# Optimization experiments

Measured on AMD Instinct MI355X. Metric: run time of the kernel, lower is better.

The kernel has to match this reference:

```python
import jax, jax.numpy as jnp
import numpy as np

D_MODEL = 1024
NUM_HEADS = 16
HEAD_DIM = D_MODEL // NUM_HEADS


def setup_inputs() -> dict:
    key = jax.random.key(0)
    ks = jax.random.split(key, 9)
    s = 1.0 / np.sqrt(D_MODEL)  # torch Linear default init range scale
    def lin(k):
        kw, kb = jax.random.split(k)
        W = jax.random.uniform(kw, (D_MODEL, D_MODEL), jnp.float32, -s, s)
        b = jax.random.uniform(kb, (D_MODEL,), jnp.float32, -s, s)
        return W, b
    Wq, bq = lin(ks[0])
    Wk, bk = lin(ks[1])
    Wv, bv = lin(ks[2])
    Wo, bo = lin(ks[3])
    x = jax.random.normal(ks[4], (4, 2048, D_MODEL), jnp.float32)
    return {"x": x, "Wq": Wq, "bq": bq, "Wk": Wk, "bk": bk,
            "Wv": Wv, "bv": bv, "Wo": Wo, "bo": bo}


def reference(x, Wq, bq, Wk, bk, Wv, bv, Wo, bo):
    B, S, _ = x.shape
    H, Dh = NUM_HEADS, HEAD_DIM
    scale = Dh ** -0.5
    # projections; W stored as [in, out] so y = x @ W + b
    q = (x @ Wq + bq).reshape(B, S, H, Dh).transpose(0, 2, 1, 3)  # [B,H,S,Dh]
    k = (x @ Wk + bk).reshape(B, S, H, Dh).transpose(0, 2, 1, 3)
    v = (x @ Wv + bv).reshape(B, S, H, Dh).transpose(0, 2, 1, 3)
    scores = jnp.einsum('bhqd,bhkd->bhqk', q, k) * scale  # [B,H,S,S]
    causal = jnp.tril(jnp.ones((S, S), dtype=bool))
    scores = jnp.where(causal[None, None], scores, jnp.finfo(scores.dtype).min)
    attn = jax.nn.softmax(scores, axis=-1)
    out = jnp.einsum('bhqk,bhkd->bhqd', attn, v)  # [B,H,S,Dh]
    out = out.transpose(0, 2, 1, 3).reshape(B, S, H * Dh)
    return out @ Wo + bo
```

## Files before the change

### kernel.cpp

```cpp
#include <hip/hip_runtime.h>
#include <math.h>

#define DM 1024
#define NH 16
#define DH 64
#define BB 4
#define SS 2048
#define MROWS (BB*SS)

typedef __bf16 bf16;
typedef __bf16 bf16x2 __attribute__((ext_vector_type(2)));
typedef __bf16 bf16x8 __attribute__((ext_vector_type(8)));
typedef float floatx4 __attribute__((ext_vector_type(4)));
typedef float floatx16 __attribute__((ext_vector_type(16)));
typedef unsigned int uintx4 __attribute__((ext_vector_type(4)));
typedef unsigned int uintx2 __attribute__((ext_vector_type(2)));

#if __has_builtin(__builtin_amdgcn_exp2f)
#define EXP2F __builtin_amdgcn_exp2f
#else
#define EXP2F exp2f
#endif

#define QSCALE (0.125f * 1.44269504088896f)

__device__ __forceinline__ void cp16(void* lds, const void* g) {
  __builtin_amdgcn_global_load_lds(
      (__attribute__((address_space(1))) void*)(void*)g,
      (__attribute__((address_space(3))) void*)lds,
      16, 0, 0);
}

__device__ __forceinline__ unsigned pk2(float a, float b) {
  bf16x2 t;
  t[0] = (bf16)a;
  t[1] = (bf16)b;
  return __builtin_bit_cast(unsigned, t);
}

#if __has_builtin(__builtin_amdgcn_permlane32_swap)
__device__ __forceinline__ void pl32(unsigned& a, unsigned& b) {
  uintx2 r = __builtin_amdgcn_permlane32_swap(a, b, false, false);
  a = r[0]; b = r[1];
}
#else
__device__ __forceinline__ void pl32(unsigned& a, unsigned& b) {
  asm volatile("v_permlane32_swap_b32 %0, %1" : "+v"(a), "+v"(b));
}
#endif

__global__ __launch_bounds__(256) void cvt_x(
    const float* __restrict__ X, bf16* __restrict__ Y) {
  int i = (blockIdx.x * 256 + threadIdx.x) * 8;
  float4 a = *(const float4*)&X[i];
  float4 b = *(const float4*)&X[i + 4];
  bf16x8 o;
  o[0] = (bf16)a.x; o[1] = (bf16)a.y; o[2] = (bf16)a.z; o[3] = (bf16)a.w;
  o[4] = (bf16)b.x; o[5] = (bf16)b.y; o[6] = (bf16)b.z; o[7] = (bf16)b.w;
  *(bf16x8*)&Y[i] = o;
}

__global__ __launch_bounds__(1024) void wtransc(
    const float* __restrict__ W0, const float* __restrict__ W1,
    const float* __restrict__ W2, const float* __restrict__ W3,
    bf16* __restrict__ T0, bf16* __restrict__ T1,
    bf16* __restrict__ T2, bf16* __restrict__ T3) {
  __shared__ float tile[32][33];
  const float* W; bf16* T;
  int z = blockIdx.z;
  if (z == 0)      { W = W0; T = T0; }
  else if (z == 1) { W = W1; T = T1; }
  else if (z == 2) { W = W2; T = T2; }
  else             { W = W3; T = T3; }
  int tx = threadIdx.x, ty = threadIdx.y;
  tile[ty][tx] = W[(blockIdx.y * 32 + ty) * DM + blockIdx.x * 32 + tx];
  __syncthreads();
  T[(blockIdx.x * 32 + ty) * DM + blockIdx.y * 32 + tx] = (bf16)tile[tx][ty];
}

#define BK 32

__global__ __launch_bounds__(512, 1) void gemm_qkv(
    const bf16* __restrict__ A, const bf16* __restrict__ WT,
    const float* __restrict__ bq, const float* __restrict__ bk,
    const float* __restrict__ bv,
    bf16* __restrict__ qb, bf16* __restrict__ kb, bf16* __restrict__ vt) {
  __shared__ __align__(16) char smem[(2 * 256 * 64 + 2 * 128 * 64) * 2];
  bf16* Ab = (bf16*)smem;
  bf16* Bb = (bf16*)(smem + 2 * 256 * 64 * 2);
  bf16* Ts = (bf16*)smem;

  int tid = threadIdx.x;
  int lane = tid & 63, w = tid >> 6;
  int wr = w >> 1, wc = w & 1;
  int qd = lane >> 4, l15 = lane & 15;

  int bid = blockIdx.x;
  int wg = (bid & 7) * 96 + (bid >> 3);
  int mb = wg / 24, nb = wg % 24;
  int m0 = mb * 256;
  int n0 = nb * 128;
  int which = n0 >> 10;

  floatx4 acc[4][4] = {};

  auto stageA = [&](int pb, int t, int hf) {
    for (int i = 0; i < 2; ++i) {
      int L = i * 512 + tid;
      int row = L >> 3, ch = L & 7;
      int sch = ch ^ (row & 7);
      cp16(&Ab[pb * 256 * 64 + (hf * 128 + row) * 64 + ch * 8],
           &A[(size_t)(m0 + hf * 128 + row) * DM + t * 64 + sch * 8]);
    }
  };
  auto stageB = [&](int pb, int t) {
    for (int i = 0; i < 2; ++i) {
      int L = i * 512 + tid;
      int row = L >> 3, ch = L & 7;
      int sch = ch ^ (row & 7);
      cp16(&Bb[pb * 128 * 64 + row * 64 + ch * 8],
           &WT[(size_t)(n0 + row) * DM + t * 64 + sch * 8]);
    }
  };
  auto ldA = [&](int pb, int mt, int ks) -> bf16x8 {
    int row = wr * 64 + mt * 16 + l15;
    int c = ((ks << 2) + qd) ^ (row & 7);
    return *(const bf16x8*)&Ab[pb * 256 * 64 + row * 64 + c * 8];
  };
  auto ldB = [&](int pb, int nt, int ks) -> bf16x8 {
    int row = wc * 64 + nt * 16 + l15;
    int c = ((ks << 2) + qd) ^ (row & 7);
    return *(const bf16x8*)&Bb[pb * 128 * 64 + row * 64 + c * 8];
  };

  stageA(0, 0, 0);
  stageA(0, 0, 1);
  stageB(0, 0);
  stageB(1, 1);
  asm volatile("s_waitcnt vmcnt(2)" ::: "memory");
  __builtin_amdgcn_s_barrier();

  for (int g = 0; g < 16; ++g) {
    int pb = g & 1;
    bf16x8 af0[2][2], bfr[4][2];
    for (int mt = 0; mt < 2; ++mt)
      for (int ks = 0; ks < 2; ++ks) af0[mt][ks] = ldA(pb, mt, ks);
    for (int nt = 0; nt < 4; ++nt)
      for (int ks = 0; ks < 2; ++ks) bfr[nt][ks] = ldB(pb, nt, ks);
    if (g + 1 < 16) { stageA(pb ^ 1, g + 1, 0); stageA(pb ^ 1, g + 1, 1); }
    __builtin_amdgcn_s_barrier();
    asm volatile("s_waitcnt lgkmcnt(0)" ::: "memory");
    __builtin_amdgcn_sched_barrier(0);
    __builtin_amdgcn_s_setprio(1);
    for (int mt = 0; mt < 2; ++mt)
      for (int nt = 0; nt < 4; ++nt)
        for (int ks = 0; ks < 2; ++ks)
          acc[mt][nt] = __builtin_amdgcn_mfma_f32_16x16x32_bf16(
              af0[mt][ks], bfr[nt][ks], acc[mt][nt], 0, 0, 0);
    __builtin_amdgcn_s_setprio(0);
    __builtin_amdgcn_s_barrier();
    bf16x8 af1[2][2];
    for (int mt = 0; mt < 2; ++mt)
      for (int ks = 0; ks < 2; ++ks) af1[mt][ks] = ldA(pb, 2 + mt, ks);
    if (g + 2 < 16) stageB(pb, g + 2);
    __builtin_amdgcn_s_barrier();
    asm volatile("s_waitcnt lgkmcnt(0)" ::: "memory");
    __builtin_amdgcn_sched_barrier(0);
    __builtin_amdgcn_s_setprio(1);
    for (int mt = 0; mt < 2; ++mt)
      for (int nt = 0; nt < 4; ++nt)
        for (int ks = 0; ks < 2; ++ks)
          acc[2 + mt][nt] = __builtin_amdgcn_mfma_f32_16x16x32_bf16(
              af1[mt][ks], bfr[nt][ks], acc[2 + mt][nt], 0, 0, 0);
    __builtin_amdgcn_s_setprio(0);
    if (g < 14)
      asm volatile("s_waitcnt vmcnt(2)" ::: "memory");
    else if (g == 14)
      asm volatile("s_waitcnt vmcnt(0)" ::: "memory");
    __builtin_amdgcn_s_barrier();
  }

  __syncthreads();

  const float* bias = (which == 0) ? bq : (which == 1) ? bk : bv;

  if (which == 2) {
    for (int nt = 0; nt < 4; ++nt) {
      int dl = wc * 64 + nt * 16 + l15;
      float bv_ = bias[(n0 & 1023) + dl];
      for (int mt = 0; mt < 4; ++mt)
        for (int r = 0; r < 4; ++r)
          Ts[dl * 264 + wr * 64 + mt * 16 + qd * 4 + r] =
              (bf16)(acc[mt][nt][r] + bv_);
    }
    __syncthreads();
    int dl = tid >> 2, s0 = (tid & 3) * 64;
    size_t vrow = (size_t)((n0 & 1023) + dl) * MROWS + m0 + s0;
    for (int j = 0; j < 8; ++j)
      *(bf16x8*)&vt[vrow + j * 8] = *(const bf16x8*)&Ts[dl * 264 + s0 + j * 8];
  } else {
    bf16* out = (which == 0) ? qb : kb;
    float sc = (which == 0) ? QSCALE : 1.0f;
    for (int nt = 0; nt < 4; ++nt) {
      int col = (n0 & 1023) + wc * 64 + nt * 16 + l15;
      float bv_ = bias[col];
      for (int mt = 0; mt < 4; ++mt)
        for (int r = 0; r < 4; ++r) {
          int row = m0 + wr * 64 + mt * 16 + qd * 4 + r;
          out[(size_t)row * DM + col] = (bf16)((acc[mt][nt][r] + bv_) * sc);
        }
    }
  }
}

__global__ __launch_bounds__(256, 4) void gemm_out(
    const bf16* __restrict__ A, const bf16* __restrict__ WT,
    const float* __restrict__ bias, float* __restrict__ C) {
  __shared__ __align__(16) bf16 As[2][64 * BK];
  __shared__ __align__(16) bf16 Bs[2][128 * BK];
  int tid = threadIdx.x;
  int lane = tid & 63, w = tid >> 6;
  int wm = (w >> 1) * 32;
  int wn = (w & 1) * 64;
  int m0 = blockIdx.x * 64;
  int n0 = blockIdx.y * 128;
  int qd = lane >> 4;
  int l15 = lane & 15;

  floatx4 acc[2][4] = {};

  auto stage = [&](int pb, int k0) {
    {
      int ci = w * 64;
      int c = ci + lane;
      int r = c >> 2, cc = (c & 3) * 8;
      cp16(&As[pb][ci * 8], &A[(size_t)(m0 + r) * DM + k0 + cc]);
    }
    for (int i = 0; i < 2; ++i) {
      int ci = (w * 2 + i) * 64;
      int c = ci + lane;
      int r = c >> 2, cc = (c & 3) * 8;
      cp16(&Bs[pb][ci * 8], &WT[(size_t)(n0 + r) * DM + k0 + cc]);
    }
  };

  stage(0, 0);
  __syncthreads();

  for (int t = 0; t < DM / BK; ++t) {
    int pb = t & 1;
    if (t + 1 < DM / BK) stage(pb ^ 1, (t + 1) * BK);
    bf16x8 af[2], bfr[4];
    for (int mt = 0; mt < 2; ++mt)
      af[mt] = *(const bf16x8*)&As[pb][(wm + mt * 16 + l15) * BK + qd * 8];
    for (int nt = 0; nt < 4; ++nt)
      bfr[nt] = *(const bf16x8*)&Bs[pb][(wn + nt * 16 + l15) * BK + qd * 8];
    for (int mt = 0; mt < 2; ++mt)
      for (int nt = 0; nt < 4; ++nt)
        acc[mt][nt] = __builtin_amdgcn_mfma_f32_16x16x32_bf16(
            af[mt], bfr[nt], acc[mt][nt], 0, 0, 0);
    __syncthreads();
  }

  for (int nt = 0; nt < 4; ++nt) {
    int col = n0 + wn + nt * 16 + l15;
    float bv = bias[col];
    for (int mt = 0; mt < 2; ++mt)
      for (int r = 0; r < 4; ++r) {
        int row = m0 + wm + mt * 16 + qd * 4 + r;
        C[(size_t)row * DM + col] = acc[mt][nt][r] + bv;
      }
  }
}

__global__ __launch_bounds__(256, 2) void attn_fwd(
    const bf16* __restrict__ Qg, const bf16* __restrict__ Kg,
    const bf16* __restrict__ Vt, bf16* __restrict__ O) {
  __shared__ __align__(16) bf16 Kbuf[3][64 * 64];
  __shared__ __align__(16) bf16 Vbuf[3][64 * 64];

  int tid = threadIdx.x;
  int lane = tid & 63, w = tid >> 6;
  int q31 = lane & 31, hi = lane >> 5;
  int pair = blockIdx.x, h = blockIdx.y, b = blockIdx.z;
  int base = b * SS;
  int hoff = h * DH;

  auto stage = [&](int bi, int kt) {
    int kbase = base + kt * 64;
    for (int i = 0; i < 2; ++i) {
      int c = i * 256 + tid;
      int row = c >> 3;
      int sch = (c & 7) ^ (row & 7);
      cp16(&Kbuf[bi][c * 8], &Kg[(size_t)(kbase + row) * DM + hoff + sch * 8]);
      cp16(&Vbuf[bi][c * 8],
           &Vt[(size_t)(hoff + row) * MROWS + base + kt * 64 + sch * 8]);
    }
  };

  int swz = q31 & 7;

  for (int ph = 0; ph < 2; ++ph) {
    int jt = ph ? (15 - pair) : pair;
    int q0 = jt * 128;
    int nkt = 2 * jt + 2;

    stage(0, 0);
    stage(1, 1);

    int rowq = q0 + w * 32 + q31;
    bf16x8 qf[4];
    for (int ds = 0; ds < 4; ++ds)
      qf[ds] = *(const bf16x8*)
          &Qg[(size_t)(base + rowq) * DM + hoff + ds * 16 + hi * 8];

    float lacc = 0.0f;
    floatx16 oacc0 = {}, oacc1 = {};

    asm volatile("s_waitcnt vmcnt(8)" ::: "memory");
    __builtin_amdgcn_s_barrier();

    int bi = 0;
    for (int kt = 0; kt < nkt; ++kt) {
      if (kt + 2 < nkt) stage((bi + 2) % 3, kt + 2);

      floatx16 sA = {}, sB = {};
      __builtin_amdgcn_s_setprio(1);
      for (int ds = 0; ds < 4; ++ds) {
        bf16x8 kfA = *(const bf16x8*)
            &Kbuf[bi][(q31)*64 + (((ds << 1) + hi) ^ swz) * 8];
        bf16x8 kfB = *(const bf16x8*)
            &Kbuf[bi][(32 + q31) * 64 + (((ds << 1) + hi) ^ swz) * 8];
        sA = __builtin_amdgcn_mfma_f32_32x32x16_bf16(kfA, qf[ds], sA, 0, 0, 0);
        sB = __builtin_amdgcn_mfma_f32_32x32x16_bf16(kfB, qf[ds], sB, 0, 0, 0);
      }
      __builtin_amdgcn_s_setprio(0);

      if (kt >= 2 * jt) {
#pragma unroll
        for (int r = 0; r < 16; ++r) {
          int key = kt * 64 + (r & 3) + 8 * (r >> 2) + 4 * hi;
          if (key > rowq) sA[r] = -3e38f;
          if (key + 32 > rowq) sB[r] = -3e38f;
        }
      }

      float pA[16], pB[16];
#pragma unroll
      for (int r = 0; r < 16; ++r) {
        pA[r] = EXP2F(sA[r]);
        pB[r] = EXP2F(sB[r]);
      }
      float s0 = 0.f, s1 = 0.f, s2 = 0.f, s3 = 0.f;
#pragma unroll
      for (int r = 0; r < 16; r += 2) {
        s0 += pA[r]; s1 += pA[r + 1];
        s2 += pB[r]; s3 += pB[r + 1];
      }
      lacc += (s0 + s1) + (s2 + s3);

      bf16x8 pf[4];
      {
        unsigned w0 = pk2(pA[0], pA[1]), w2 = pk2(pA[4], pA[5]);
        unsigned w1 = pk2(pA[2], pA[3]), w3 = pk2(pA[6], pA[7]);
        pl32(w0, w2); pl32(w1, w3);
        uintx4 ww; ww[0] = w0; ww[1] = w1; ww[2] = w2; ww[3] = w3;
        pf[0] = __builtin_bit_cast(bf16x8, ww);
        w0 = pk2(pA[8], pA[9]);  w2 = pk2(pA[12], pA[13]);
        w1 = pk2(pA[10], pA[11]); w3 = pk2(pA[14], pA[15]);
        pl32(w0, w2); pl32(w1, w3);
        ww[0] = w0; ww[1] = w1; ww[2] = w2; ww[3] = w3;
        pf[1] = __builtin_bit_cast(bf16x8, ww);
        w0 = pk2(pB[0], pB[1]);  w2 = pk2(pB[4], pB[5]);
        w1 = pk2(pB[2], pB[3]);  w3 = pk2(pB[6], pB[7]);
        pl32(w0, w2); pl32(w1, w3);
        ww[0] = w0; ww[1] = w1; ww[2] = w2; ww[3] = w3;
        pf[2] = __builtin_bit_cast(bf16x8, ww);
        w0 = pk2(pB[8], pB[9]);  w2 = pk2(pB[12], pB[13]);
        w1 = pk2(pB[10], pB[11]); w3 = pk2(pB[14], pB[15]);
        pl32(w0, w2); pl32(w1, w3);
        ww[0] = w0; ww[1] = w1; ww[2] = w2; ww[3] = w3;
        pf[3] = __builtin_bit_cast(bf16x8, ww);
      }

      __builtin_amdgcn_s_setprio(1);
#pragma unroll
      for (int s4 = 0; s4 < 4; ++s4) {
        bf16x8 vf0 = *(const bf16x8*)
            &Vbuf[bi][(q31)*64 + (((s4 << 1) + hi) ^ swz) * 8];
        bf16x8 vf1 = *(const bf16x8*)
            &Vbuf[bi][(32 + q31) * 64 + (((s4 << 1) + hi) ^ swz) * 8];
        oacc0 = __builtin_amdgcn_mfma_f32_32x32x16_bf16(pf[s4], vf0, oacc0, 0, 0, 0);
        oacc1 = __builtin_amdgcn_mfma_f32_32x32x16_bf16(pf[s4], vf1, oacc1, 0, 0, 0);
      }
      __builtin_amdgcn_s_setprio(0);

      int rem = nkt - 1 - kt;
      if (rem >= 2) {
        asm volatile("s_waitcnt vmcnt(8)" ::: "memory");
        __builtin_amdgcn_s_barrier();
      } else if (rem == 1) {
        asm volatile("s_waitcnt vmcnt(0)" ::: "memory");
        __builtin_amdgcn_s_barrier();
      }
      bi = (bi == 2) ? 0 : bi + 1;
    }

    __syncthreads();

    lacc += __shfl_xor(lacc, 32, 64);
#pragma unroll
    for (int r = 0; r < 16; ++r) {
      int rr = (r & 3) + 8 * (r >> 2) + 4 * hi;
      float inv = 1.0f / __shfl(lacc, rr, 64);
      size_t row = (size_t)(base + q0 + w * 32 + rr) * DM + hoff;
      O[row + q31] = (bf16)(oacc0[r] * inv);
      O[row + 32 + q31] = (bf16)(oacc1[r] * inv);
    }
  }
}

extern "C" void kernel_launch(void* const* d_in, const int* in_sizes, int n_in,
                              void* d_out, int out_size, void* d_ws, size_t ws_size,
                              hipStream_t stream) {
  const float* x  = (const float*)d_in[0];
  const float* Wq = (const float*)d_in[1];
  const float* bq = (const float*)d_in[2];
  const float* Wk = (const float*)d_in[3];
  const float* bk = (const float*)d_in[4];
  const float* Wv = (const float*)d_in[5];
  const float* bv = (const float*)d_in[6];
  const float* Wo = (const float*)d_in[7];
  const float* bo = (const float*)d_in[8];
  float* out = (float*)d_out;

  char* ws = (char*)d_ws;
  const size_t act = (size_t)MROWS * DM * sizeof(bf16);
  bf16* xb    = (bf16*)(ws);
  bf16* qb    = (bf16*)(ws + act);
  bf16* kb    = (bf16*)(ws + 2 * act);
  bf16* vt    = (bf16*)(ws + 3 * act);
  bf16* ab    = (bf16*)(ws + 4 * act);
  bf16* WqkvT = (bf16*)(ws + 5 * act);
  bf16* WoT   = WqkvT + 3 * (size_t)DM * DM;

  cvt_x<<<MROWS * DM / (256 * 8), 256, 0, stream>>>(x, xb);
  wtransc<<<dim3(32, 32, 4), dim3(32, 32), 0, stream>>>(
      Wq, Wk, Wv, Wo,
      WqkvT, WqkvT + (size_t)DM * DM, WqkvT + 2 * (size_t)DM * DM, WoT);

  gemm_qkv<<<768, 512, 0, stream>>>(
      xb, WqkvT, bq, bk, bv, qb, kb, vt);

  attn_fwd<<<dim3(8, NH, BB), 256, 0, stream>>>(qb, kb, vt, ab);

  gemm_out<<<dim3(128, 8), 256, 0, stream>>>(ab, WoT, bo, out);
}
```

Measured before the change: 260.3 us.

## Port output projection GEMM to 256x128 pipelined tile scheme and remap QKV blocks

Rewrites the output-projection GEMM to use the same 512-thread, 256x128 tile, XOR-swizzled LDS, split A/B staging pipeline with barriers and priority hints that the QKV GEMM already uses, replacing the small 64x128 BK=32 kernel. It also changes the QKV GEMM's block-to-tile mapping so that each XCD gets a fixed set of N-column tiles. Larger tiles are meant to cut global reloads and improve MFMA density. The cost is one block per CU and only 256 blocks for the output GEMM, which may leave some CUs idle on the second wave.

```diff
diff --git a/kernel.cpp b/kernel.cpp
--- a/kernel.cpp
+++ b/kernel.cpp
@@ -96,8 +96,8 @@
   int qd = lane >> 4, l15 = lane & 15;
 
   int bid = blockIdx.x;
-  int wg = (bid & 7) * 96 + (bid >> 3);
-  int mb = wg / 24, nb = wg % 24;
+  int xcd = bid & 7, rr_ = bid >> 3;
+  int mb = rr_ & 31, nb = xcd * 3 + (rr_ >> 5);
   int m0 = mb * 256;
   int n0 = nb * 128;
   int which = n0 >> 10;
@@ -213,62 +213,107 @@
   }
 }
 
-__global__ __launch_bounds__(256, 4) void gemm_out(
+__global__ __launch_bounds__(512, 1) void gemm_out(
     const bf16* __restrict__ A, const bf16* __restrict__ WT,
     const float* __restrict__ bias, float* __restrict__ C) {
-  __shared__ __align__(16) bf16 As[2][64 * BK];
-  __shared__ __align__(16) bf16 Bs[2][128 * BK];
+  __shared__ __align__(16) char smem[(2 * 256 * 64 + 2 * 128 * 64) * 2];
+  bf16* Ab = (bf16*)smem;
+  bf16* Bb = (bf16*)(smem + 2 * 256 * 64 * 2);
+
   int tid = threadIdx.x;
   int lane = tid & 63, w = tid >> 6;
-  int wm = (w >> 1) * 32;
-  int wn = (w & 1) * 64;
-  int m0 = blockIdx.x * 64;
-  int n0 = blockIdx.y * 128;
-  int qd = lane >> 4;
-  int l15 = lane & 15;
-
-  floatx4 acc[2][4] = {};
-
-  auto stage = [&](int pb, int k0) {
-    {
-      int ci = w * 64;
-      int c = ci + lane;
-      int r = c >> 2, cc = (c & 3) * 8;
-      cp16(&As[pb][ci * 8], &A[(size_t)(m0 + r) * DM + k0 + cc]);
-    }
+  int wr = w >> 1, wc = w & 1;
+  int qd = lane >> 4, l15 = lane & 15;
+
+  int bid = blockIdx.x;
+  int m0 = (bid >> 3) * 256;
+  int n0 = (bid & 7) * 128;
+
+  floatx4 acc[4][4] = {};
+
+  auto stageA = [&](int pb, int t, int hf) {
     for (int i = 0; i < 2; ++i) {
-      int ci = (w * 2 + i) * 64;
-      int c = ci + lane;
-      int r = c >> 2, cc = (c & 3) * 8;
-      cp16(&Bs[pb][ci * 8], &WT[(size_t)(n0 + r) * DM + k0 + cc]);
-    }
-  };
-
-  stage(0, 0);
-  __syncthreads();
-
-  for (int t = 0; t < DM / BK; ++t) {
-    int pb = t & 1;
-    if (t + 1 < DM / BK) stage(pb ^ 1, (t + 1) * BK);
-    bf16x8 af[2], bfr[4];
-    for (int mt = 0; mt < 2; ++mt)
-      af[mt] = *(const bf16x8*)&As[pb][(wm + mt * 16 + l15) * BK + qd * 8];
+      int L = i * 512 + tid;
+      int row = L >> 3, ch = L & 7;
+      int sch = ch ^ (row & 7);
+      cp16(&Ab[pb * 256 * 64 + (hf * 128 + row) * 64 + ch * 8],
+           &A[(size_t)(m0 + hf * 128 + row) * DM + t * 64 + sch * 8]);
+    }
+  };
+  auto stageB = [&](int pb, int t) {
+    for (int i = 0; i < 2; ++i) {
+      int L = i * 512 + tid;
+      int row = L >> 3, ch = L & 7;
+      int sch = ch ^ (row & 7);
+      cp16(&Bb[pb * 128 * 64 + row * 64 + ch * 8],
+           &WT[(size_t)(n0 + row) * DM + t * 64 + sch * 8]);
+    }
+  };
+  auto ldA = [&](int pb, int mt, int ks) -> bf16x8 {
+    int row = wr * 64 + mt * 16 + l15;
+    int c = ((ks << 2) + qd) ^ (row & 7);
+    return *(const bf16x8*)&Ab[pb * 256 * 64 + row * 64 + c * 8];
+  };
+  auto ldB = [&](int pb, int nt, int ks) -> bf16x8 {
+    int row = wc * 64 + nt * 16 + l15;
+    int c = ((ks << 2) + qd) ^ (row & 7);
+    return *(const bf16x8*)&Bb[pb * 128 * 64 + row * 64 + c * 8];
+  };
+
+  stageA(0, 0, 0);
+  stageA(0, 0, 1);
+  stageB(0, 0);
+  stageB(1, 1);
+  asm volatile("s_waitcnt vmcnt(2)" ::: "memory");
+  __builtin_amdgcn_s_barrier();
+
+  for (int g = 0; g < 16; ++g) {
+    int pb = g & 1;
+    bf16x8 af0[2][2], bfr[4][2];
+    for (int mt = 0; mt < 2; ++mt)
+      for (int ks = 0; ks < 2; ++ks) af0[mt][ks] = ldA(pb, mt, ks);
     for (int nt = 0; nt < 4; ++nt)
-      bfr[nt] = *(const bf16x8*)&Bs[pb][(wn + nt * 16 + l15) * BK + qd * 8];
+      for (int ks = 0; ks < 2; ++ks) bfr[nt][ks] = ldB(pb, nt, ks);
+    if (g + 1 < 16) { stageA(pb ^ 1, g + 1, 0); stageA(pb ^ 1, g + 1, 1); }
+    __builtin_amdgcn_s_barrier();
+    asm volatile("s_waitcnt lgkmcnt(0)" ::: "memory");
+    __builtin_amdgcn_sched_barrier(0);
+    __builtin_amdgcn_s_setprio(1);
     for (int mt = 0; mt < 2; ++mt)
       for (int nt = 0; nt < 4; ++nt)
-        acc[mt][nt] = __builtin_amdgcn_mfma_f32_16x16x32_bf16(
-            af[mt], bfr[nt], acc[mt][nt], 0, 0, 0);
-    __syncthreads();
+        for (int ks = 0; ks < 2; ++ks)
+          acc[mt][nt] = __builtin_amdgcn_mfma_f32_16x16x32_bf16(
+              af0[mt][ks], bfr[nt][ks], acc[mt][nt], 0, 0, 0);
+    __builtin_amdgcn_s_setprio(0);
+    __builtin_amdgcn_s_barrier();
+    bf16x8 af1[2][2];
+    for (int mt = 0; mt < 2; ++mt)
+      for (int ks = 0; ks < 2; ++ks) af1[mt][ks] = ldA(pb, 2 + mt, ks);
+    if (g + 2 < 16) stageB(pb, g + 2);
+    __builtin_amdgcn_s_barrier();
+    asm volatile("s_waitcnt lgkmcnt(0)" ::: "memory");
+    __builtin_amdgcn_sched_barrier(0);
+    __builtin_amdgcn_s_setprio(1);
+    for (int mt = 0; mt < 2; ++mt)
+      for (int nt = 0; nt < 4; ++nt)
+        for (int ks = 0; ks < 2; ++ks)
+          acc[2 + mt][nt] = __builtin_amdgcn_mfma_f32_16x16x32_bf16(
+              af1[mt][ks], bfr[nt][ks], acc[2 + mt][nt], 0, 0, 0);
+    __builtin_amdgcn_s_setprio(0);
+    if (g < 14)
+      asm volatile("s_waitcnt vmcnt(2)" ::: "memory");
+    else if (g == 14)
+      asm volatile("s_waitcnt vmcnt(0)" ::: "memory");
+    __builtin_amdgcn_s_barrier();
   }
 
   for (int nt = 0; nt < 4; ++nt) {
-    int col = n0 + wn + nt * 16 + l15;
-    float bv = bias[col];
-    for (int mt = 0; mt < 2; ++mt)
+    int col = n0 + wc * 64 + nt * 16 + l15;
+    float bv_ = bias[col];
+    for (int mt = 0; mt < 4; ++mt)
       for (int r = 0; r < 4; ++r) {
-        int row = m0 + wm + mt * 16 + qd * 4 + r;
-        C[(size_t)row * DM + col] = acc[mt][nt][r] + bv;
+        int row = m0 + wr * 64 + mt * 16 + qd * 4 + r;
+        C[(size_t)row * DM + col] = acc[mt][nt][r] + bv_;
       }
   }
 }
@@ -454,5 +499,5 @@
 
   attn_fwd<<<dim3(8, NH, BB), 256, 0, stream>>>(qb, kb, vt, ab);
 
-  gemm_out<<<dim3(128, 8), 256, 0, stream>>>(ab, WoT, bo, out);
-}
+  gemm_out<<<256, 512, 0, stream>>>(ab, WoT, bo, out);
+}
```

Result: slower. 274.2 us (+5.3%).
